# Optimization experiments

Hardware: AMD Instinct MI355X
Metric: run time of the kernel (lower is better)

Reference implementation:

```python
import jax, jax.numpy as jnp
import numpy as np

N_NODES = 50000
N_EDGES = 800000
NUM_IN, NUM_HID, NUM_OUT = 512, 256, 64
EPS = 1e-12


def agnn_conv(x, src, dst, beta, num_nodes):
    # PyG AGNNConv: score(j->i) = beta * cos(x_i, x_j); softmax over incoming
    # edges of each target node i; out_i = sum_j alpha_ij * x_j.
    norm = jnp.maximum(jnp.linalg.norm(x, axis=1, keepdims=True), EPS)
    xn = x / norm                                      # [N, H]
    scores = beta * jnp.sum(xn[dst] * xn[src], axis=1)  # [E]
    m = jax.ops.segment_max(scores, dst, num_segments=num_nodes)
    e = jnp.exp(scores - m[dst])
    s = jax.ops.segment_sum(e, dst, num_segments=num_nodes)
    alpha = e / s[dst]                                  # [E]
    return jax.ops.segment_sum(alpha[:, None] * x[src], dst, num_segments=num_nodes)


def setup_inputs() -> dict:
    key = jax.random.key(0)
    ks = jax.random.split(key, 7)
    x = jax.random.normal(ks[0], (N_NODES, NUM_IN), dtype=jnp.float32)
    edge_index = jax.random.randint(ks[1], (2, N_EDGES), 0, N_NODES, dtype=jnp.int64)
    w1 = jax.random.normal(ks[2], (NUM_HID, NUM_IN), dtype=jnp.float32) / np.sqrt(NUM_IN)
    b1 = jnp.zeros((NUM_HID,), dtype=jnp.float32)
    beta2 = jnp.ones((1,), dtype=jnp.float32)
    w2 = jax.random.normal(ks[3], (NUM_OUT, NUM_HID), dtype=jnp.float32) / np.sqrt(NUM_HID)
    b2 = jnp.zeros((NUM_OUT,), dtype=jnp.float32)
    return {"x": x, "edge_index": edge_index, "w1": w1, "b1": b1,
            "beta2": beta2, "w2": w2, "b2": b2}


def reference(x, edge_index, w1, b1, beta2, w2, b2):
    n = x.shape[0]
    # add self-loops (PyG AGNNConv default add_self_loops=True)
    loops = jnp.arange(n, dtype=edge_index.dtype)
    src = jnp.concatenate([edge_index[0], loops])
    dst = jnp.concatenate([edge_index[1], loops])

    h = jax.nn.relu(x @ w1.T + b1)                       # [N, H] (eval: dropout = id)
    h = agnn_conv(h, src, dst, jnp.float32(1.0), n)      # prop1, fixed beta=1
    z1 = h
    h = agnn_conv(h, src, dst, beta2[0], n)              # prop2, learnable beta
    z2 = h
    logits = h @ w2.T + b2                               # [N, C]
    return (z1, z2, jax.nn.log_softmax(logits, axis=1))
```

## Files before the change

kernel.cpp:

```cpp
#include <hip/hip_runtime.h>

#define N_NODES 50000
#define N_EDGES 800000
#define ETOT (N_EDGES + N_NODES)
#define DIN 512
#define HID 256
#define NOUT 64
#define SCAN_CHUNK 2048

typedef __attribute__((ext_vector_type(8))) short short8;
typedef __attribute__((ext_vector_type(4))) float f32x4;
typedef __attribute__((ext_vector_type(4))) unsigned short us4;
typedef __attribute__((ext_vector_type(4))) unsigned int u32x4;

__device__ __forceinline__ unsigned short f2bf(float f) {
  union { float f; unsigned u; } x; x.f = f;
  unsigned r = x.u + 0x7fff + ((x.u >> 16) & 1);
  return (unsigned short)(r >> 16);
}
__device__ __forceinline__ float bf2f(unsigned short b) {
  return __uint_as_float(((unsigned)b) << 16);
}
__device__ __forceinline__ unsigned cvtpk(float a, float b) {
  unsigned r;
  asm("v_cvt_pk_bf16_f32 %0, %1, %2" : "=v"(r) : "v"(a), "v"(b));
  return r;
}

#define AS1(p) ((const __attribute__((address_space(1))) unsigned int*)(p))
#define AS3(p) ((__attribute__((address_space(3))) unsigned int*)(p))

__device__ __forceinline__ int edge_at(const void* ei, long long idx, int is32) {
  if (is32) return ((const int*)ei)[idx];
  return (int)((const long long*)ei)[idx];
}

__global__ void initK(const void* ei, int* cursor, int* flag,
                      const float* __restrict__ w1, unsigned short* __restrict__ wb) {
  int i = blockIdx.x * blockDim.x + threadIdx.x;
  if (i < N_NODES) cursor[i] = 1;
  if (i < (HID * DIN) / 8) {
    const float* src = w1 + i * 8;
    float4 v0 = ((const float4*)src)[0];
    float4 v1 = ((const float4*)src)[1];
    short8 s;
    s[0] = f2bf(v0.x); s[1] = f2bf(v0.y); s[2] = f2bf(v0.z); s[3] = f2bf(v0.w);
    s[4] = f2bf(v1.x); s[5] = f2bf(v1.y); s[6] = f2bf(v1.z); s[7] = f2bf(v1.w);
    *(short8*)(wb + i * 8) = s;
  }
  if (blockIdx.x == 0 && threadIdx.x < 64) {
    int lane = threadIdx.x;
    bool bad = false;
#pragma unroll
    for (int j = 0; j < 32; ++j) {
      long long v = ((const long long*)ei)[lane * 32 + j];
      bad |= (v < 0 || v >= N_NODES);
    }
    bool anybad = __any(bad);
    if (lane == 0) *flag = anybad ? 1 : 0;
  }
}

__global__ void histK(const void* ei, const int* flag, int* cursor) {
  int e = blockIdx.x * blockDim.x + threadIdx.x;
  if (e >= N_EDGES) return;
  int f = *flag;
  int d = edge_at(ei, (long long)N_EDGES + e, f);
  atomicAdd(&cursor[d], 1);
}

__global__ void scan1K(const int* counts, int* excl, int* bsums) {
  __shared__ int sdata[256];
  int base = blockIdx.x * SCAN_CHUNK;
  int t = threadIdx.x;
  int local[8];
  int sum = 0;
#pragma unroll
  for (int j = 0; j < 8; ++j) {
    int idx = base + t * 8 + j;
    int v = (idx < N_NODES) ? counts[idx] : 0;
    local[j] = sum;
    sum += v;
  }
  sdata[t] = sum;
  __syncthreads();
  for (int off = 1; off < 256; off <<= 1) {
    int v = (t >= off) ? sdata[t - off] : 0;
    __syncthreads();
    sdata[t] += v;
    __syncthreads();
  }
  int texcl = (t == 0) ? 0 : sdata[t - 1];
#pragma unroll
  for (int j = 0; j < 8; ++j) {
    int idx = base + t * 8 + j;
    if (idx < N_NODES) excl[idx] = texcl + local[j];
  }
  if (t == 255) bsums[blockIdx.x] = sdata[255];
}

__global__ void scan3K(int* row_ptr, const int* bsums, int* cursor) {
  int i = blockIdx.x * blockDim.x + threadIdx.x;
  if (i < N_NODES) {
    int nb = i >> 11;
    int pre = 0;
    for (int b = 0; b < nb; ++b) pre += bsums[b];
    int v = row_ptr[i] + pre;
    row_ptr[i] = v;
    cursor[i] = v;
    if (i == 0) row_ptr[N_NODES] = ETOT;
  }
}

__global__ void scatterK(const void* ei, const int* flag, int* cursor, int* col) {
  int e = blockIdx.x * blockDim.x + threadIdx.x;
  if (e < N_EDGES) {
    int f = *flag;
    int s = edge_at(ei, e, f);
    int d = edge_at(ei, (long long)N_EDGES + e, f);
    int pos = atomicAdd(&cursor[d], 1);
    col[pos] = s;
  } else if (e < N_EDGES + N_NODES) {
    int i = e - N_EDGES;
    int pos = atomicAdd(&cursor[i], 1);
    col[pos] = i;
  }
}

__global__ __launch_bounds__(256) void gemm1MF(const float* __restrict__ A,
                                               const unsigned short* __restrict__ Bb,
                                               const float* __restrict__ bias,
                                               unsigned short* __restrict__ C,
                                               float* __restrict__ invn) {
  __shared__ float As[64 * 64];
  __shared__ short Bs[256 * 64];
  int t = threadIdx.x;
  int wv = t >> 6, ln = t & 63;
  int wc = wv;
  int row0 = blockIdx.x * 64;

  const float* aptr[4];
#pragma unroll
  for (int i = 0; i < 4; ++i) {
    int chunk = i * 4 + wv;
    int r = chunk * 4 + (ln >> 4);
    int gr = row0 + r;
    if (gr >= N_NODES) gr = N_NODES - 1;
    aptr[i] = &A[(long long)gr * DIN + (((ln & 15) ^ (r & 7)) << 2)];
  }
  const unsigned short* bptr[8];
#pragma unroll
  for (int i = 0; i < 8; ++i) {
    int chunk = i * 4 + wv;
    int r = chunk * 8 + (ln >> 3);
    bptr[i] = &Bb[(long long)r * DIN + (((ln & 7) ^ (r & 7)) << 3)];
  }

  f32x4 acc[4][4];
#pragma unroll
  for (int mi = 0; mi < 4; ++mi)
#pragma unroll
    for (int ni = 0; ni < 4; ++ni) acc[mi][ni] = (f32x4){0.f, 0.f, 0.f, 0.f};

  int g = ln >> 4;
  int fr = ln & 15;

  for (int k0 = 0; k0 < DIN; k0 += 64) {
#pragma unroll
    for (int i = 0; i < 4; ++i)
      __builtin_amdgcn_global_load_lds(AS1(aptr[i] + k0),
                                       AS3(&As[(i * 4 + wv) * 256]), 16, 0, 0);
#pragma unroll
    for (int i = 0; i < 8; ++i)
      __builtin_amdgcn_global_load_lds(AS1(bptr[i] + k0),
                                       AS3(&Bs[(i * 4 + wv) * 512]), 16, 0, 0);
    __syncthreads();

#pragma unroll
    for (int kk = 0; kk < 2; ++kk) {
      short8 af[4], bfr[4];
#pragma unroll
      for (int mi = 0; mi < 4; ++mi) {
        int r = mi * 16 + fr;
        int s0 = kk * 8 + ((2 * g) ^ (r & 7));
        int s1 = kk * 8 + ((2 * g + 1) ^ (r & 7));
        f32x4 a0 = *(const f32x4*)&As[r * 64 + s0 * 4];
        f32x4 a1 = *(const f32x4*)&As[r * 64 + s1 * 4];
        u32x4 pk;
        pk.x = cvtpk(a0[0], a0[1]);
        pk.y = cvtpk(a0[2], a0[3]);
        pk.z = cvtpk(a1[0], a1[1]);
        pk.w = cvtpk(a1[2], a1[3]);
        af[mi] = __builtin_bit_cast(short8, pk);
      }
#pragma unroll
      for (int ni = 0; ni < 4; ++ni) {
        int c = wc * 64 + ni * 16 + fr;
        int slot = (kk * 4 + g) ^ (c & 7);
        bfr[ni] = *(const short8*)&Bs[c * 64 + slot * 8];
      }
#pragma unroll
      for (int mi = 0; mi < 4; ++mi)
#pragma unroll
        for (int ni = 0; ni < 4; ++ni)
          acc[mi][ni] = __builtin_amdgcn_mfma_f32_16x16x32_bf16(af[mi], bfr[ni], acc[mi][ni], 0, 0, 0);
    }
    __syncthreads();
  }

  int fq = ln >> 4;
  float ss[4][4];
#pragma unroll
  for (int mi = 0; mi < 4; ++mi)
#pragma unroll
    for (int j = 0; j < 4; ++j) ss[mi][j] = 0.f;

#pragma unroll
  for (int ni = 0; ni < 4; ++ni) {
    int colv = wc * 64 + ni * 16 + fr;
    float bv = bias[colv];
#pragma unroll
    for (int mi = 0; mi < 4; ++mi) {
#pragma unroll
      for (int j = 0; j < 4; ++j) {
        int row = row0 + mi * 16 + fq * 4 + j;
        unsigned short us = f2bf(fmaxf(acc[mi][ni][j] + bv, 0.f));
        if (row < N_NODES) C[(long long)row * HID + colv] = us;
        float v = bf2f(us);
        ss[mi][j] = fmaf(v, v, ss[mi][j]);
      }
    }
  }

#pragma unroll
  for (int mi = 0; mi < 4; ++mi)
#pragma unroll
    for (int j = 0; j < 4; ++j) {
      float s = ss[mi][j];
      s += __shfl_xor(s, 1);
      s += __shfl_xor(s, 2);
      s += __shfl_xor(s, 4);
      s += __shfl_xor(s, 8);
      ss[mi][j] = s;
    }
  float* redS = As;
  if (fr == 0) {
#pragma unroll
    for (int mi = 0; mi < 4; ++mi)
#pragma unroll
      for (int j = 0; j < 4; ++j)
        redS[(mi * 16 + fq * 4 + j) * 4 + wv] = ss[mi][j];
  }
  __syncthreads();
  if (t < 64) {
    int row = row0 + t;
    if (row < N_NODES) {
      float tot = redS[t * 4 + 0] + redS[t * 4 + 1] + redS[t * 4 + 2] + redS[t * 4 + 3];
      invn[row] = 1.0f / fmaxf(sqrtf(tot), 1e-12f);
    }
  }
}

__global__ __launch_bounds__(256) void convK(const unsigned short* __restrict__ hb,
                                             const float* __restrict__ invn,
                                             const int* __restrict__ row_ptr,
                                             const int* __restrict__ col,
                                             const float* __restrict__ beta_ptr,
                                             float* __restrict__ hout,
                                             unsigned short* __restrict__ hout_bf,
                                             float* __restrict__ invn_out) {
  int w = (blockIdx.x * 256 + threadIdx.x) >> 6;
  int lane = threadIdx.x & 63;
  if (w >= N_NODES) return;
  int g = lane >> 4;
  int sub = lane & 15;
  float beta = beta_ptr ? beta_ptr[0] : 1.0f;
  float babs = fabsf(beta);

  const unsigned short* hrow = &hb[(long long)w * HID + sub * 16];
  short8 hia = *(const short8*)hrow;
  short8 hib = *(const short8*)(hrow + 8);
  float hi[16];
#pragma unroll
  for (int q = 0; q < 8; ++q) {
    hi[q] = bf2f((unsigned short)hia[q]);
    hi[8 + q] = bf2f((unsigned short)hib[q]);
  }
  float scale_i = invn[w] * beta;

  int e0 = row_ptr[w], e1 = row_ptr[w + 1];
  int nit = (e1 - e0 + 3) >> 2;
  float Z = 0.f;
  float acc[16];
#pragma unroll
  for (int q = 0; q < 16; ++q) acc[q] = 0.f;

  for (int it = 0; it < nit; ++it) {
    int ee = e0 + it * 4 + g;
    bool valid = ee < e1;
    int s = col[valid ? ee : (e1 - 1)];
    float is = invn[s];
    const unsigned short* hj = &hb[(long long)s * HID + sub * 16];
    short8 ja = *(const short8*)hj;
    short8 jb = *(const short8*)(hj + 8);
    float hjf[16];
#pragma unroll
    for (int q = 0; q < 8; ++q) {
      hjf[q] = bf2f((unsigned short)ja[q]);
      hjf[8 + q] = bf2f((unsigned short)jb[q]);
    }
    float p = 0.f;
#pragma unroll
    for (int q = 0; q < 16; ++q) p += hi[q] * hjf[q];
    p += __shfl_xor(p, 1);
    p += __shfl_xor(p, 2);
    p += __shfl_xor(p, 4);
    p += __shfl_xor(p, 8);
    float sc = p * scale_i * is;
    float wt = valid ? __expf(sc - babs) : 0.f;
    Z += wt;
#pragma unroll
    for (int q = 0; q < 16; ++q) acc[q] += wt * hjf[q];
  }

#pragma unroll
  for (int q = 0; q < 16; ++q) {
    acc[q] += __shfl_xor(acc[q], 16);
    acc[q] += __shfl_xor(acc[q], 32);
  }
  Z += __shfl_xor(Z, 16);
  Z += __shfl_xor(Z, 32);
  float r = 1.0f / Z;

  if (g == 0) {
    float* po = &hout[(long long)w * HID + sub * 16];
#pragma unroll
    for (int q4 = 0; q4 < 4; ++q4) {
      float4 o;
      o.x = acc[q4 * 4 + 0] * r;
      o.y = acc[q4 * 4 + 1] * r;
      o.z = acc[q4 * 4 + 2] * r;
      o.w = acc[q4 * 4 + 3] * r;
      *(float4*)&po[q4 * 4] = o;
    }
  } else if (g == 1 && hout_bf) {
    unsigned short* pb = &hout_bf[(long long)w * HID + sub * 16];
#pragma unroll
    for (int q4 = 0; q4 < 4; ++q4) {
      us4 ob;
      ob.x = f2bf(acc[q4 * 4 + 0] * r);
      ob.y = f2bf(acc[q4 * 4 + 1] * r);
      ob.z = f2bf(acc[q4 * 4 + 2] * r);
      ob.w = f2bf(acc[q4 * 4 + 3] * r);
      *(us4*)&pb[q4 * 4] = ob;
    }
  }

  if (invn_out) {
    float ss = 0.f;
#pragma unroll
    for (int q = 0; q < 16; ++q) {
      float v = bf2f(f2bf(acc[q] * r));
      ss = fmaf(v, v, ss);
    }
    ss += __shfl_xor(ss, 1);
    ss += __shfl_xor(ss, 2);
    ss += __shfl_xor(ss, 4);
    ss += __shfl_xor(ss, 8);
    if (lane == 0) invn_out[w] = 1.0f / fmaxf(sqrtf(ss), 1e-12f);
  }
}

__global__ __launch_bounds__(256) void headK2(const float* __restrict__ Z,
                                              const float* __restrict__ W,
                                              const float* __restrict__ bias,
                                              float* __restrict__ out) {
  __shared__ float smem[2 * 32 * 68];
  float* As = smem;
  float* Bs = smem + 32 * 68;
  int t = threadIdx.x;
  int tx = t & 15, ty = t >> 4;
  int row0 = blockIdx.x * 64;
  float acc[4][4] = {};
  int lr = t >> 3;
  int lc4 = t & 7;

  for (int k0 = 0; k0 < HID; k0 += 32) {
#pragma unroll
    for (int rr = 0; rr < 64; rr += 32) {
      int gr = row0 + lr + rr;
      float4 va = (gr < N_NODES)
                      ? *(const float4*)&Z[(long long)gr * HID + k0 + lc4 * 4]
                      : make_float4(0.f, 0.f, 0.f, 0.f);
      As[(lc4 * 4 + 0) * 68 + lr + rr] = va.x;
      As[(lc4 * 4 + 1) * 68 + lr + rr] = va.y;
      As[(lc4 * 4 + 2) * 68 + lr + rr] = va.z;
      As[(lc4 * 4 + 3) * 68 + lr + rr] = va.w;
      int gc = lr + rr;
      float4 vb = *(const float4*)&W[(long long)gc * HID + k0 + lc4 * 4];
      Bs[(lc4 * 4 + 0) * 68 + lr + rr] = vb.x;
      Bs[(lc4 * 4 + 1) * 68 + lr + rr] = vb.y;
      Bs[(lc4 * 4 + 2) * 68 + lr + rr] = vb.z;
      Bs[(lc4 * 4 + 3) * 68 + lr + rr] = vb.w;
    }
    __syncthreads();
#pragma unroll
    for (int kk = 0; kk < 32; ++kk) {
      float4 a4 = *(const float4*)&As[kk * 68 + ty * 4];
      float4 b4 = *(const float4*)&Bs[kk * 68 + tx * 4];
      acc[0][0] += a4.x * b4.x; acc[0][1] += a4.x * b4.y; acc[0][2] += a4.x * b4.z; acc[0][3] += a4.x * b4.w;
      acc[1][0] += a4.y * b4.x; acc[1][1] += a4.y * b4.y; acc[1][2] += a4.y * b4.z; acc[1][3] += a4.y * b4.w;
      acc[2][0] += a4.z * b4.x; acc[2][1] += a4.z * b4.y; acc[2][2] += a4.z * b4.z; acc[2][3] += a4.z * b4.w;
      acc[3][0] += a4.w * b4.x; acc[3][1] += a4.w * b4.y; acc[3][2] += a4.w * b4.z; acc[3][3] += a4.w * b4.w;
    }
    __syncthreads();
  }

  float* ls = smem;
  float4 bv = *(const float4*)&bias[tx * 4];
#pragma unroll
  for (int r = 0; r < 4; ++r) {
    int lrow = ty * 4 + r;
    ls[lrow * 65 + tx * 4 + 0] = acc[r][0] + bv.x;
    ls[lrow * 65 + tx * 4 + 1] = acc[r][1] + bv.y;
    ls[lrow * 65 + tx * 4 + 2] = acc[r][2] + bv.z;
    ls[lrow * 65 + tx * 4 + 3] = acc[r][3] + bv.w;
  }
  __syncthreads();

  int wid = t >> 6, lane = t & 63;
#pragma unroll
  for (int rr2 = wid; rr2 < 64; rr2 += 4) {
    int node = row0 + rr2;
    if (node < N_NODES) {
      float v = ls[rr2 * 65 + lane];
      float mx = v;
#pragma unroll
      for (int off = 32; off >= 1; off >>= 1) mx = fmaxf(mx, __shfl_xor(mx, off));
      float ex = __expf(v - mx);
      float se = ex;
#pragma unroll
      for (int off = 32; off >= 1; off >>= 1) se += __shfl_xor(se, off);
      out[(long long)node * NOUT + lane] = v - mx - __logf(se);
    }
  }
}

extern "C" void kernel_launch(void* const* d_in, const int* in_sizes, int n_in,
                              void* d_out, int out_size, void* d_ws, size_t ws_size,
                              hipStream_t stream) {
  (void)in_sizes; (void)n_in; (void)out_size; (void)ws_size;
  const float* x = (const float*)d_in[0];
  const void* ei = d_in[1];
  const float* w1 = (const float*)d_in[2];
  const float* b1 = (const float*)d_in[3];
  const float* beta2 = (const float*)d_in[4];
  const float* w2 = (const float*)d_in[5];
  const float* b2 = (const float*)d_in[6];

  float* z1 = (float*)d_out;
  float* z2 = z1 + (size_t)N_NODES * HID;
  float* lsm = z2 + (size_t)N_NODES * HID;

  unsigned short* h_bf = (unsigned short*)d_ws;
  unsigned short* z1_bf = h_bf + (size_t)N_NODES * HID;
  float* invn = (float*)(z1_bf + (size_t)N_NODES * HID);
  int* row_ptr = (int*)(invn + N_NODES);
  int* cursor = row_ptr + N_NODES + 1;
  int* colv = cursor + N_NODES;
  int* bsums = colv + ETOT;
  int* flag = bsums + 64;
  unsigned short* wb = (unsigned short*)(flag + 4);
  float* invn2 = (float*)(wb + (size_t)HID * DIN);

  int nScan = (N_NODES + SCAN_CHUNK - 1) / SCAN_CHUNK;

  initK<<<(N_NODES + 255) / 256, 256, 0, stream>>>(ei, cursor, flag, w1, wb);

  gemm1MF<<<(N_NODES + 63) / 64, 256, 0, stream>>>(x, wb, b1, h_bf, invn);

  histK<<<(N_EDGES + 255) / 256, 256, 0, stream>>>(ei, flag, cursor);
  scan1K<<<nScan, 256, 0, stream>>>(cursor, row_ptr, bsums);
  scan3K<<<(N_NODES + 255) / 256, 256, 0, stream>>>(row_ptr, bsums, cursor);
  scatterK<<<(N_EDGES + N_NODES + 255) / 256, 256, 0, stream>>>(ei, flag, cursor, colv);

  convK<<<(N_NODES + 3) / 4, 256, 0, stream>>>(h_bf, invn, row_ptr, colv, nullptr, z1, z1_bf, invn2);
  convK<<<(N_NODES + 3) / 4, 256, 0, stream>>>(z1_bf, invn2, row_ptr, colv, beta2, z2, nullptr, nullptr);

  headK2<<<(N_NODES + 63) / 64, 256, 0, stream>>>(z2, w2, b2, lsm);
}
```

Before: 333.2 us.

## Fuse second AGNN propagation with output linear head and log-softmax

Replaces the second convK launch and the separate tiled FP32 head GEMM with one kernel. It computes the attention aggregation per node in a wavefront, then applies the bf16 W2 projection from LDS and the log-softmax in registers. W2 is pre-packed to bf16 pairs in initK. This removes one launch and the re-read of z2 from global memory. In exchange the head uses bf16 weights, every block reloads 32KB of W2 into LDS, and register pressure rises.

```diff
diff --git a/kernel.cpp b/kernel.cpp
--- a/kernel.cpp
+++ b/kernel.cpp
@@ -10,8 +10,11 @@
 
 typedef __attribute__((ext_vector_type(8))) short short8;
 typedef __attribute__((ext_vector_type(4))) float f32x4;
+typedef __attribute__((ext_vector_type(2))) float f32x2;
 typedef __attribute__((ext_vector_type(4))) unsigned short us4;
 typedef __attribute__((ext_vector_type(4))) unsigned int u32x4;
+
+#define FMA2(a, b, c) __builtin_elementwise_fma((a), (b), (c))
 
 __device__ __forceinline__ unsigned short f2bf(float f) {
   union { float f; unsigned u; } x; x.f = f;
@@ -21,6 +24,12 @@
 __device__ __forceinline__ float bf2f(unsigned short b) {
   return __uint_as_float(((unsigned)b) << 16);
 }
+__device__ __forceinline__ f32x2 bfpair(unsigned u) {
+  f32x2 r;
+  r.x = __uint_as_float(u << 16);
+  r.y = __uint_as_float(u & 0xffff0000u);
+  return r;
+}
 __device__ __forceinline__ unsigned cvtpk(float a, float b) {
   unsigned r;
   asm("v_cvt_pk_bf16_f32 %0, %1, %2" : "=v"(r) : "v"(a), "v"(b));
@@ -36,7 +45,8 @@
 }
 
 __global__ void initK(const void* ei, int* cursor, int* flag,
-                      const float* __restrict__ w1, unsigned short* __restrict__ wb) {
+                      const float* __restrict__ w1, unsigned short* __restrict__ wb,
+                      const float* __restrict__ w2, unsigned* __restrict__ w2b) {
   int i = blockIdx.x * blockDim.x + threadIdx.x;
   if (i < N_NODES) cursor[i] = 1;
   if (i < (HID * DIN) / 8) {
@@ -47,6 +57,13 @@
     s[0] = f2bf(v0.x); s[1] = f2bf(v0.y); s[2] = f2bf(v0.z); s[3] = f2bf(v0.w);
     s[4] = f2bf(v1.x); s[5] = f2bf(v1.y); s[6] = f2bf(v1.z); s[7] = f2bf(v1.w);
     *(short8*)(wb + i * 8) = s;
+  }
+  if (i < (NOUT * HID) / 2) {
+    int c = i >> 7, kp = i & 127;
+    const float* wr = w2 + c * HID + kp * 2;
+    unsigned lo = f2bf(wr[0]);
+    unsigned hi = f2bf(wr[1]);
+    w2b[i] = lo | (hi << 16);
   }
   if (blockIdx.x == 0 && threadIdx.x < 64) {
     int lane = threadIdx.x;
@@ -371,79 +388,130 @@
   }
 }
 
-__global__ __launch_bounds__(256) void headK2(const float* __restrict__ Z,
-                                              const float* __restrict__ W,
-                                              const float* __restrict__ bias,
-                                              float* __restrict__ out) {
-  __shared__ float smem[2 * 32 * 68];
-  float* As = smem;
-  float* Bs = smem + 32 * 68;
+__global__ __launch_bounds__(256) void convHeadK(const unsigned short* __restrict__ hb,
+                                                 const float* __restrict__ invn,
+                                                 const int* __restrict__ row_ptr,
+                                                 const int* __restrict__ col,
+                                                 const float* __restrict__ beta_ptr,
+                                                 const unsigned* __restrict__ w2b,
+                                                 const float* __restrict__ b2,
+                                                 float* __restrict__ hout,
+                                                 float* __restrict__ lsm) {
+  __shared__ unsigned w2s[NOUT * 128];
   int t = threadIdx.x;
-  int tx = t & 15, ty = t >> 4;
-  int row0 = blockIdx.x * 64;
-  float acc[4][4] = {};
-  int lr = t >> 3;
-  int lc4 = t & 7;
-
-  for (int k0 = 0; k0 < HID; k0 += 32) {
-#pragma unroll
-    for (int rr = 0; rr < 64; rr += 32) {
-      int gr = row0 + lr + rr;
-      float4 va = (gr < N_NODES)
-                      ? *(const float4*)&Z[(long long)gr * HID + k0 + lc4 * 4]
-                      : make_float4(0.f, 0.f, 0.f, 0.f);
-      As[(lc4 * 4 + 0) * 68 + lr + rr] = va.x;
-      As[(lc4 * 4 + 1) * 68 + lr + rr] = va.y;
-      As[(lc4 * 4 + 2) * 68 + lr + rr] = va.z;
-      As[(lc4 * 4 + 3) * 68 + lr + rr] = va.w;
-      int gc = lr + rr;
-      float4 vb = *(const float4*)&W[(long long)gc * HID + k0 + lc4 * 4];
-      Bs[(lc4 * 4 + 0) * 68 + lr + rr] = vb.x;
-      Bs[(lc4 * 4 + 1) * 68 + lr + rr] = vb.y;
-      Bs[(lc4 * 4 + 2) * 68 + lr + rr] = vb.z;
-      Bs[(lc4 * 4 + 3) * 68 + lr + rr] = vb.w;
-    }
-    __syncthreads();
-#pragma unroll
-    for (int kk = 0; kk < 32; ++kk) {
-      float4 a4 = *(const float4*)&As[kk * 68 + ty * 4];
-      float4 b4 = *(const float4*)&Bs[kk * 68 + tx * 4];
-      acc[0][0] += a4.x * b4.x; acc[0][1] += a4.x * b4.y; acc[0][2] += a4.x * b4.z; acc[0][3] += a4.x * b4.w;
-      acc[1][0] += a4.y * b4.x; acc[1][1] += a4.y * b4.y; acc[1][2] += a4.y * b4.z; acc[1][3] += a4.y * b4.w;
-      acc[2][0] += a4.z * b4.x; acc[2][1] += a4.z * b4.y; acc[2][2] += a4.z * b4.z; acc[2][3] += a4.z * b4.w;
-      acc[3][0] += a4.w * b4.x; acc[3][1] += a4.w * b4.y; acc[3][2] += a4.w * b4.z; acc[3][3] += a4.w * b4.w;
-    }
-    __syncthreads();
-  }
-
-  float* ls = smem;
-  float4 bv = *(const float4*)&bias[tx * 4];
-#pragma unroll
-  for (int r = 0; r < 4; ++r) {
-    int lrow = ty * 4 + r;
-    ls[lrow * 65 + tx * 4 + 0] = acc[r][0] + bv.x;
-    ls[lrow * 65 + tx * 4 + 1] = acc[r][1] + bv.y;
-    ls[lrow * 65 + tx * 4 + 2] = acc[r][2] + bv.z;
-    ls[lrow * 65 + tx * 4 + 3] = acc[r][3] + bv.w;
-  }
+#pragma unroll
+  for (int i = 0; i < 32; ++i) w2s[i * 256 + t] = w2b[i * 256 + t];
   __syncthreads();
 
-  int wid = t >> 6, lane = t & 63;
-#pragma unroll
-  for (int rr2 = wid; rr2 < 64; rr2 += 4) {
-    int node = row0 + rr2;
-    if (node < N_NODES) {
-      float v = ls[rr2 * 65 + lane];
-      float mx = v;
-#pragma unroll
-      for (int off = 32; off >= 1; off >>= 1) mx = fmaxf(mx, __shfl_xor(mx, off));
-      float ex = __expf(v - mx);
-      float se = ex;
-#pragma unroll
-      for (int off = 32; off >= 1; off >>= 1) se += __shfl_xor(se, off);
-      out[(long long)node * NOUT + lane] = v - mx - __logf(se);
-    }
-  }
+  int w = (blockIdx.x * 256 + t) >> 6;
+  int lane = t & 63;
+  int g = lane >> 4;
+  int sub = lane & 15;
+  float beta = beta_ptr[0];
+  float babs = fabsf(beta);
+
+  const unsigned short* hrow = &hb[(long long)w * HID + sub * 16];
+  short8 hia = *(const short8*)hrow;
+  short8 hib = *(const short8*)(hrow + 8);
+  float hi[16];
+#pragma unroll
+  for (int q = 0; q < 8; ++q) {
+    hi[q] = bf2f((unsigned short)hia[q]);
+    hi[8 + q] = bf2f((unsigned short)hib[q]);
+  }
+  float scale_i = invn[w] * beta;
+
+  int e0 = row_ptr[w], e1 = row_ptr[w + 1];
+  int nit = (e1 - e0 + 3) >> 2;
+  float Z = 0.f;
+  float acc[16];
+#pragma unroll
+  for (int q = 0; q < 16; ++q) acc[q] = 0.f;
+
+  for (int it = 0; it < nit; ++it) {
+    int ee = e0 + it * 4 + g;
+    bool valid = ee < e1;
+    int s = col[valid ? ee : (e1 - 1)];
+    float is = invn[s];
+    const unsigned short* hj = &hb[(long long)s * HID + sub * 16];
+    short8 ja = *(const short8*)hj;
+    short8 jb = *(const short8*)(hj + 8);
+    float hjf[16];
+#pragma unroll
+    for (int q = 0; q < 8; ++q) {
+      hjf[q] = bf2f((unsigned short)ja[q]);
+      hjf[8 + q] = bf2f((unsigned short)jb[q]);
+    }
+    float p = 0.f;
+#pragma unroll
+    for (int q = 0; q < 16; ++q) p += hi[q] * hjf[q];
+    p += __shfl_xor(p, 1);
+    p += __shfl_xor(p, 2);
+    p += __shfl_xor(p, 4);
+    p += __shfl_xor(p, 8);
+    float sc = p * scale_i * is;
+    float wt = valid ? __expf(sc - babs) : 0.f;
+    Z += wt;
+#pragma unroll
+    for (int q = 0; q < 16; ++q) acc[q] += wt * hjf[q];
+  }
+
+#pragma unroll
+  for (int q = 0; q < 16; ++q) {
+    acc[q] += __shfl_xor(acc[q], 16);
+    acc[q] += __shfl_xor(acc[q], 32);
+  }
+  Z += __shfl_xor(Z, 16);
+  Z += __shfl_xor(Z, 32);
+  float r = 1.0f / Z;
+
+  if (g == 0) {
+    float* po = &hout[(long long)w * HID + sub * 16];
+#pragma unroll
+    for (int q4 = 0; q4 < 4; ++q4) {
+      float4 o;
+      o.x = acc[q4 * 4 + 0] * r;
+      o.y = acc[q4 * 4 + 1] * r;
+      o.z = acc[q4 * 4 + 2] * r;
+      o.w = acc[q4 * 4 + 3] * r;
+      *(float4*)&po[q4 * 4] = o;
+    }
+  }
+
+  f32x2 zp[8];
+#pragma unroll
+  for (int j2 = 0; j2 < 8; ++j2)
+    zp[j2] = (f32x2){acc[2 * j2] * r, acc[2 * j2 + 1] * r};
+
+  float p[16];
+#pragma unroll
+  for (int idx = 0; idx < 16; ++idx) {
+    int c = g * 16 + idx;
+    const unsigned* wrow = &w2s[c * 128 + sub * 8];
+    f32x2 d = (f32x2){0.f, 0.f};
+#pragma unroll
+    for (int j2 = 0; j2 < 8; ++j2) d = FMA2(bfpair(wrow[j2]), zp[j2], d);
+    p[idx] = d.x + d.y;
+  }
+#pragma unroll
+  for (int m = 1; m <= 8; m <<= 1) {
+#pragma unroll
+    for (int idx = 0; idx < 16; ++idx) p[idx] += __shfl_xor(p[idx], m);
+  }
+  float logit = 0.f;
+#pragma unroll
+  for (int idx = 0; idx < 16; ++idx)
+    if (sub == idx) logit = p[idx];
+  logit += b2[lane];
+
+  float mx = logit;
+#pragma unroll
+  for (int off = 1; off <= 32; off <<= 1) mx = fmaxf(mx, __shfl_xor(mx, off));
+  float ex = __expf(logit - mx);
+  float se = ex;
+#pragma unroll
+  for (int off = 1; off <= 32; off <<= 1) se += __shfl_xor(se, off);
+  lsm[(long long)w * NOUT + lane] = logit - mx - __logf(se);
 }
 
 extern "C" void kernel_launch(void* const* d_in, const int* in_sizes, int n_in,
@@ -472,10 +540,11 @@
   int* flag = bsums + 64;
   unsigned short* wb = (unsigned short*)(flag + 4);
   float* invn2 = (float*)(wb + (size_t)HID * DIN);
+  unsigned* w2b = (unsigned*)(invn2 + N_NODES);
 
   int nScan = (N_NODES + SCAN_CHUNK - 1) / SCAN_CHUNK;
 
-  initK<<<(N_NODES + 255) / 256, 256, 0, stream>>>(ei, cursor, flag, w1, wb);
+  initK<<<(N_NODES + 255) / 256, 256, 0, stream>>>(ei, cursor, flag, w1, wb, w2, w2b);
 
   gemm1MF<<<(N_NODES + 63) / 64, 256, 0, stream>>>(x, wb, b1, h_bf, invn);
 
@@ -485,7 +554,5 @@
   scatterK<<<(N_EDGES + N_NODES + 255) / 256, 256, 0, stream>>>(ei, flag, cursor, colv);
 
   convK<<<(N_NODES + 3) / 4, 256, 0, stream>>>(h_bf, invn, row_ptr, colv, nullptr, z1, z1_bf, invn2);
-  convK<<<(N_NODES + 3) / 4, 256, 0, stream>>>(z1_bf, invn2, row_ptr, colv, beta2, z2, nullptr, nullptr);
-
-  headK2<<<(N_NODES + 63) / 64, 256, 0, stream>>>(z2, w2, b2, lsm);
-}
+  convHeadK<<<(N_NODES + 3) / 4, 256, 0, stream>>>(z1_bf, invn2, row_ptr, colv, beta2, w2b, b2, z2, lsm);
+}
```

Measured after the change: 356.5 us. 7.0% more time.
